# Optimization experiments

Measured on AMD Instinct MI355X. Metric: run time of the kernel, lower is better.

Reference implementation:

```python
import jax, jax.numpy as jnp
import numpy as np

NDIR = 6      # build_tree.num_directions()
IDIM = 256
ODIM = 512
B, L, NCH = 8, 4096, 8192


def setup_inputs() -> dict:
    key = jax.random.key(0)
    ks = jax.random.split(key, 9)
    last = jax.random.normal(ks[0], (B, NCH, IDIM), dtype=jnp.float32)
    child_l = jax.random.randint(ks[1], (L,), 0, NCH, dtype=jnp.int32)
    child_r = jax.random.randint(ks[2], (L,), 0, NCH, dtype=jnp.int32)
    vec = jax.random.randint(ks[3], (B, L), 0, NCH, dtype=jnp.int32)
    drev = jax.random.randint(ks[4], (NCH,), 0, 2, dtype=jnp.int32)
    dmap = jax.random.randint(ks[5], (NCH,), 0, NDIR, dtype=jnp.int32)
    # merge FC params: ndir independent Linear(2*idim -> odim) + PReLU(init=relu_weight)
    scale = 1.0 / np.sqrt(2 * IDIM)
    W_merge = jax.random.uniform(ks[6], (NDIR, ODIM, 2 * IDIM), jnp.float32, -scale, scale)
    b_merge = jax.random.uniform(ks[7], (NDIR, ODIM), jnp.float32, -scale, scale)
    alpha_merge = jnp.full((NDIR,), 0.005, dtype=jnp.float32)  # PReLU weight (relu_weight)
    return {"last": last, "W_merge": W_merge, "b_merge": b_merge,
            "alpha_merge": alpha_merge, "child_l": child_l, "child_r": child_r,
            "vec": vec, "drev": drev, "dmap": dmap}


def reference(last, W_merge, b_merge, alpha_merge, child_l, child_r, vec, drev, dmap):
    # child gathers: [B, L, idim]
    lch = last[:, child_l]
    rch = last[:, child_r]
    # per-element direction-reverse blending
    d = drev[vec][:, :, None].astype(last.dtype)          # [B, L, 1]
    a = lch * (1.0 - d) + rch * d
    b = rch * (1.0 - d) + lch * d
    ans = jnp.concatenate([a, b], axis=-1)                # [B, L, 2*idim]
    # routed merge: compute all ndir linears, then select per element (ndir is small)
    y_all = jnp.einsum('bli,doi->bldo', ans, W_merge) + b_merge   # [B, L, ndir, odim]
    dir_idx = dmap[vec]                                   # [B, L] in [0, ndir)
    y = jnp.take_along_axis(y_all, dir_idx[:, :, None, None], axis=2)[:, :, 0]  # [B, L, odim]
    alpha = alpha_merge[dir_idx][:, :, None]              # per-element PReLU slope
    return jnp.where(y > 0, y, alpha * y)
```

## Files before the change

### kernel.cpp

```cpp
#include <hip/hip_runtime.h>
#include <hip/hip_bf16.h>

#define BB 8
#define LL 4096
#define NCH 8192
#define IDIM 256
#define KDIM 512
#define ODIM 512
#define NDIR 6
#define TOT (BB * LL)

typedef short short8 __attribute__((ext_vector_type(8)));
typedef float floatx4 __attribute__((ext_vector_type(4)));

#define WS_LAST_OFF (64 + 2 * TOT)
#define LAST_ELEMS (BB * NCH * IDIM)
#define W_ELEMS (NDIR * ODIM * KDIM)
#define N_LAST8 (LAST_ELEMS / 8)
#define N_W8 (W_ELEMS / 8)

#define GEMM_CHUNK 131

__device__ inline void async_copy16(const void* g, void* l) {
  __builtin_amdgcn_global_load_lds(
      (const __attribute__((address_space(1))) void*)g,
      (__attribute__((address_space(3))) void*)l, 16, 0, 0);
}

__device__ inline void cvt8(const float* __restrict__ src,
                            __hip_bfloat16* __restrict__ dst, int i) {
  const floatx4* s = (const floatx4*)src;
  floatx4 a = s[2 * i];
  floatx4 b = s[2 * i + 1];
  union { short8 v; __hip_bfloat16 h[8]; } u;
  u.h[0] = __float2bfloat16(a[0]); u.h[1] = __float2bfloat16(a[1]);
  u.h[2] = __float2bfloat16(a[2]); u.h[3] = __float2bfloat16(a[3]);
  u.h[4] = __float2bfloat16(b[0]); u.h[5] = __float2bfloat16(b[1]);
  u.h[6] = __float2bfloat16(b[2]); u.h[7] = __float2bfloat16(b[3]);
  ((short8*)dst)[i] = u.v;
}

__global__ __launch_bounds__(256) void prep_kernel(
    const float* __restrict__ last, const float* __restrict__ W,
    const int* __restrict__ vec, const int* __restrict__ dmap,
    int* __restrict__ ws) {
  __hip_bfloat16* last_bf = (__hip_bfloat16*)(ws + WS_LAST_OFF);
  __hip_bfloat16* W_bf = last_bf + LAST_ELEMS;
  int gid = blockIdx.x * 256 + threadIdx.x;
  if (gid < N_LAST8) {
    cvt8(last, last_bf, gid);
  } else if (gid < N_LAST8 + N_W8) {
    cvt8(W, W_bf, gid - N_LAST8);
  } else {
    __shared__ int lcnt[8];
    int tid = threadIdx.x;
    if (tid < 8) lcnt[tid] = 0;
    __syncthreads();
    int lin = gid - (N_LAST8 + N_W8);
    int dir = dmap[vec[lin]] & 7;
    atomicAdd(&lcnt[dir], 1);
    __syncthreads();
    if (tid < 8 && lcnt[tid]) atomicAdd(&ws[tid], lcnt[tid]);
  }
}

__global__ __launch_bounds__(256) void scatter_kernel(
    const int* __restrict__ vec, const int* __restrict__ child_l,
    const int* __restrict__ child_r, const int* __restrict__ drev,
    const int* __restrict__ dmap, int* __restrict__ ws) {
  __shared__ int lcnt[8];
  __shared__ int gbase[8];
  __shared__ int baseS[8];
  int* fill = ws + 8;
  int* idx = ws + 64;
  int* rows = ws + 64 + TOT;

  int tid = threadIdx.x;
  if (tid < 8) {
    lcnt[tid] = 0;
    int s = 0;
    for (int i = 0; i < tid; ++i) s += ws[i];
    baseS[tid] = s;
  }
  __syncthreads();

  int lin = blockIdx.x * 256 + tid;
  int l = lin & (LL - 1);
  int v = vec[lin];
  int dir = dmap[v] & 7;
  int sw = drev[v];
  int cl = child_l[l];
  int cr = child_r[l];
  int r0 = sw ? cr : cl;
  int r1 = sw ? cl : cr;
  int pos = atomicAdd(&lcnt[dir], 1);
  __syncthreads();
  if (tid < 8) gbase[tid] = lcnt[tid] ? atomicAdd(&fill[tid], lcnt[tid]) : 0;
  __syncthreads();
  int slot = baseS[dir] + gbase[dir] + pos;
  idx[slot] = lin;
  rows[slot] = r0 | (r1 << 16);
}

__global__ __launch_bounds__(256) void gemm_kernel(
    const float* __restrict__ bias, const float* __restrict__ alpha_m,
    const int* __restrict__ ws, float* __restrict__ out) {
  __shared__ __hip_bfloat16 Als[2][128 * 64];

  int flat = blockIdx.y * 4 + blockIdx.x;
  int swz = (flat & 7) * GEMM_CHUNK + (flat >> 3);
  const int mt = swz >> 2;
  const int nt = swz & 3;

  int d = -1, count = 0, off = 0, m_base = 0;
  {
    int tb = 0, run = 0;
    for (int dd = 0; dd < NDIR; ++dd) {
      int c = ws[dd];
      int ntile = (c + 127) >> 7;
      if (mt < tb + ntile) { d = dd; count = c; off = run; m_base = (mt - tb) * 128; break; }
      tb += ntile; run += c;
    }
  }
  if (d < 0) return;

  const int* idx = ws + 64;
  const int* rows = ws + 64 + TOT;
  const __hip_bfloat16* last_bf = (const __hip_bfloat16*)(ws + WS_LAST_OFF);
  const __hip_bfloat16* W_bf = last_bf + LAST_ELEMS;

  const int tid = threadIdx.x;
  const int wave = __builtin_amdgcn_readfirstlane(tid >> 6);
  const int lane = tid & 63;
  const int lane15 = lane & 15;
  const int quad = lane >> 4;
  const int wm = wave >> 1;
  const int wn = wave & 1;
  const int n_blk = nt * 128;

  const __hip_bfloat16* ap0[4];
  const __hip_bfloat16* ap1[4];
  int ldsrow[4];
#pragma unroll
  for (int i = 0; i < 4; ++i) {
    int sr = wave * 32 + i * 8 + (lane >> 3);
    ldsrow[i] = (wave * 32 + i * 8) * 64;
    int lr = m_base + sr;
    if (lr >= count) lr = count - 1;
    int lin = idx[off + lr] & (TOT - 1);
    int rr = rows[off + lr];
    int b = lin >> 12;
    int r0 = rr & (NCH - 1);
    int r1 = (rr >> 16) & (NCH - 1);
    int xu = ((lane & 7) ^ (sr & 7)) * 8;
    ap0[i] = last_bf + (long long)(b * NCH + r0) * IDIM + xu;
    ap1[i] = last_bf + (long long)(b * NCH + r1) * IDIM + xu;
  }
  const __hip_bfloat16* bp[4];
#pragma unroll
  for (int j = 0; j < 4; ++j)
    bp[j] = W_bf + (long long)(d * ODIM + n_blk + wn * 64 + j * 16 + lane15) * KDIM + quad * 8;

  floatx4 acc[4][4] = {};
  const int lx = lane15 & 7;

#pragma unroll
  for (int i = 0; i < 4; ++i) async_copy16(ap0[i], &Als[0][ldsrow[i]]);
  __syncthreads();

#pragma unroll
  for (int kt = 0; kt < 8; ++kt) {
    const int cur = kt & 1;
    short8 bfr[2][4];
#pragma unroll
    for (int s = 0; s < 2; ++s)
#pragma unroll
      for (int j = 0; j < 4; ++j)
        bfr[s][j] = *(const short8*)(bp[j] + kt * 64 + s * 32);

    if (kt < 7) {
      const int tn = kt + 1;
      const int ko = (tn & 3) * 64;
#pragma unroll
      for (int i = 0; i < 4; ++i) {
        const __hip_bfloat16* ga = (tn < 4 ? ap0[i] : ap1[i]) + ko;
        async_copy16(ga, &Als[cur ^ 1][ldsrow[i]]);
      }
    }

#pragma unroll
    for (int s = 0; s < 2; ++s) {
      const int xcol = ((quad + 4 * s) ^ lx) * 8;
      short8 a[4];
#pragma unroll
      for (int i = 0; i < 4; ++i)
        a[i] = *(const short8*)&Als[cur][(wm * 64 + i * 16 + lane15) * 64 + xcol];
#pragma unroll
      for (int i = 0; i < 4; ++i)
#pragma unroll
        for (int j = 0; j < 4; ++j)
          acc[i][j] = __builtin_amdgcn_mfma_f32_16x16x32_bf16(a[i], bfr[s][j], acc[i][j], 0, 0, 0);
    }
    __syncthreads();
  }

  const float alpha = alpha_m[d];
  float bj[4];
#pragma unroll
  for (int j = 0; j < 4; ++j)
    bj[j] = bias[d * ODIM + n_blk + wn * 64 + j * 16 + lane15];

#pragma unroll
  for (int i = 0; i < 4; ++i) {
#pragma unroll
    for (int reg = 0; reg < 4; ++reg) {
      int row_id = m_base + wm * 64 + i * 16 + quad * 4 + reg;
      if (row_id >= count) continue;
      int lin = idx[off + row_id] & (TOT - 1);
      float* orow = out + (long long)lin * ODIM + n_blk + wn * 64;
#pragma unroll
      for (int j = 0; j < 4; ++j) {
        float y = acc[i][j][reg] + bj[j];
        y = y > 0.f ? y : alpha * y;
        orow[j * 16 + lane15] = y;
      }
    }
  }
}

extern "C" void kernel_launch(void* const* d_in, const int* in_sizes, int n_in,
                              void* d_out, int out_size, void* d_ws, size_t ws_size,
                              hipStream_t stream) {
  const float* last = (const float*)d_in[0];
  const float* W = (const float*)d_in[1];
  const float* bias = (const float*)d_in[2];
  const float* alpha = (const float*)d_in[3];
  const int* child_l = (const int*)d_in[4];
  const int* child_r = (const int*)d_in[5];
  const int* vec = (const int*)d_in[6];
  const int* drev = (const int*)d_in[7];
  const int* dmap = (const int*)d_in[8];

  int* ws = (int*)d_ws;

  hipMemsetAsync(ws, 0, 64 * sizeof(int), stream);
  int prep_blocks = (N_LAST8 + N_W8 + TOT) / 256;
  prep_kernel<<<prep_blocks, 256, 0, stream>>>(last, W, vec, dmap, ws);
  scatter_kernel<<<TOT / 256, 256, 0, stream>>>(vec, child_l, child_r, drev, dmap, ws);
  dim3 grid(ODIM / 128, TOT / 128 + NDIR, 1);
  gemm_kernel<<<grid, 256, 0, stream>>>(bias, alpha, ws, (float*)d_out);
}
```

Baseline: 184.2 us.

## Fuse scatter into prep with per-direction buckets and use single-wave GEMM tiles

Drops the separate scatter kernel by having prep directly write index/row pairs into fixed-capacity per-direction buckets (CAP slots each), so no prefix sum over counts is needed. The GEMM switches to 64-thread single-wave blocks computing 64x64 tiles, with explicit s_waitcnt-based double buffering in place of __syncthreads. The aim is to save a launch and barrier overhead and to get more, smaller tiles for load balance. In exchange each tile reuses less data, and the code assumes no direction ever exceeds CAP entries.

```diff
diff --git a/kernel.cpp b/kernel.cpp
--- a/kernel.cpp
+++ b/kernel.cpp
@@ -10,16 +10,18 @@
 #define NDIR 6
 #define TOT (BB * LL)
 
-typedef short short8 __attribute__((ext_vector_type(8)));
-typedef float floatx4 __attribute__((ext_vector_type(4)));
-
-#define WS_LAST_OFF (64 + 2 * TOT)
+#define CAP 8192
+#define IDX_OFF 64
+#define ROWS_OFF (64 + 8 * CAP)
+#define WS_LAST_OFF (64 + 16 * CAP)
 #define LAST_ELEMS (BB * NCH * IDIM)
 #define W_ELEMS (NDIR * ODIM * KDIM)
 #define N_LAST8 (LAST_ELEMS / 8)
 #define N_W8 (W_ELEMS / 8)
 
-#define GEMM_CHUNK 131
+#define MTILES (TOT / 64 + NDIR)
+typedef short short8 __attribute__((ext_vector_type(8)));
+typedef float floatx4 __attribute__((ext_vector_type(4)));
 
 __device__ inline void async_copy16(const void* g, void* l) {
   __builtin_amdgcn_global_load_lds(
@@ -42,8 +44,9 @@
 
 __global__ __launch_bounds__(256) void prep_kernel(
     const float* __restrict__ last, const float* __restrict__ W,
-    const int* __restrict__ vec, const int* __restrict__ dmap,
-    int* __restrict__ ws) {
+    const int* __restrict__ vec, const int* __restrict__ child_l,
+    const int* __restrict__ child_r, const int* __restrict__ drev,
+    const int* __restrict__ dmap, int* __restrict__ ws) {
   __hip_bfloat16* last_bf = (__hip_bfloat16*)(ws + WS_LAST_OFF);
   __hip_bfloat16* W_bf = last_bf + LAST_ELEMS;
   int gid = blockIdx.x * 256 + threadIdx.x;
@@ -53,140 +56,107 @@
     cvt8(W, W_bf, gid - N_LAST8);
   } else {
     __shared__ int lcnt[8];
+    __shared__ int gbase[8];
     int tid = threadIdx.x;
     if (tid < 8) lcnt[tid] = 0;
     __syncthreads();
     int lin = gid - (N_LAST8 + N_W8);
-    int dir = dmap[vec[lin]] & 7;
-    atomicAdd(&lcnt[dir], 1);
+    int l = lin & (LL - 1);
+    int v = vec[lin];
+    int dir = dmap[v] & 7;
+    int sw = drev[v];
+    int cl = child_l[l];
+    int cr = child_r[l];
+    int r0 = sw ? cr : cl;
+    int r1 = sw ? cl : cr;
+    int pos = atomicAdd(&lcnt[dir], 1);
     __syncthreads();
-    if (tid < 8 && lcnt[tid]) atomicAdd(&ws[tid], lcnt[tid]);
-  }
-}
-
-__global__ __launch_bounds__(256) void scatter_kernel(
-    const int* __restrict__ vec, const int* __restrict__ child_l,
-    const int* __restrict__ child_r, const int* __restrict__ drev,
-    const int* __restrict__ dmap, int* __restrict__ ws) {
-  __shared__ int lcnt[8];
-  __shared__ int gbase[8];
-  __shared__ int baseS[8];
-  int* fill = ws + 8;
-  int* idx = ws + 64;
-  int* rows = ws + 64 + TOT;
-
-  int tid = threadIdx.x;
-  if (tid < 8) {
-    lcnt[tid] = 0;
-    int s = 0;
-    for (int i = 0; i < tid; ++i) s += ws[i];
-    baseS[tid] = s;
-  }
-  __syncthreads();
-
-  int lin = blockIdx.x * 256 + tid;
-  int l = lin & (LL - 1);
-  int v = vec[lin];
-  int dir = dmap[v] & 7;
-  int sw = drev[v];
-  int cl = child_l[l];
-  int cr = child_r[l];
-  int r0 = sw ? cr : cl;
-  int r1 = sw ? cl : cr;
-  int pos = atomicAdd(&lcnt[dir], 1);
-  __syncthreads();
-  if (tid < 8) gbase[tid] = lcnt[tid] ? atomicAdd(&fill[tid], lcnt[tid]) : 0;
-  __syncthreads();
-  int slot = baseS[dir] + gbase[dir] + pos;
-  idx[slot] = lin;
-  rows[slot] = r0 | (r1 << 16);
-}
-
-__global__ __launch_bounds__(256) void gemm_kernel(
+    if (tid < 8) gbase[tid] = lcnt[tid] ? atomicAdd(&ws[tid], lcnt[tid]) : 0;
+    __syncthreads();
+    int slot = dir * CAP + gbase[dir] + pos;
+    ws[IDX_OFF + slot] = lin;
+    ws[ROWS_OFF + slot] = r0 | (r1 << 16);
+  }
+}
+
+__global__ __launch_bounds__(64) void gemm_kernel(
     const float* __restrict__ bias, const float* __restrict__ alpha_m,
     const int* __restrict__ ws, float* __restrict__ out) {
-  __shared__ __hip_bfloat16 Als[2][128 * 64];
-
-  int flat = blockIdx.y * 4 + blockIdx.x;
-  int swz = (flat & 7) * GEMM_CHUNK + (flat >> 3);
-  const int mt = swz >> 2;
-  const int nt = swz & 3;
-
-  int d = -1, count = 0, off = 0, m_base = 0;
+  __shared__ __hip_bfloat16 Als[2][64 * 64];
+
+  int flat = blockIdx.y * 8 + blockIdx.x;
+  int swz = (flat & 7) * MTILES + (flat >> 3);
+  const int mt = swz >> 3;
+  const int nt = swz & 7;
+
+  int d = -1, count = 0, m_base = 0;
   {
-    int tb = 0, run = 0;
-    for (int dd = 0; dd < NDIR; ++dd) {
+    int tb = 0;
+    for (int dd = 0; dd < 8; ++dd) {
       int c = ws[dd];
-      int ntile = (c + 127) >> 7;
-      if (mt < tb + ntile) { d = dd; count = c; off = run; m_base = (mt - tb) * 128; break; }
-      tb += ntile; run += c;
+      int ntile = (c + 63) >> 6;
+      if (mt < tb + ntile) { d = dd; count = c; m_base = (mt - tb) * 64; break; }
+      tb += ntile;
     }
   }
   if (d < 0) return;
 
-  const int* idx = ws + 64;
-  const int* rows = ws + 64 + TOT;
-  const __hip_bfloat16* last_bf = (const __hip_bfloat16*)(ws + WS_LAST_OFF);
-  const __hip_bfloat16* W_bf = last_bf + LAST_ELEMS;
-
-  const int tid = threadIdx.x;
-  const int wave = __builtin_amdgcn_readfirstlane(tid >> 6);
-  const int lane = tid & 63;
+  const int* idxA = ws + IDX_OFF + d * CAP;
+  const int* rowsA = ws + ROWS_OFF + d * CAP;
+  const char* last_bf = (const char*)(ws + WS_LAST_OFF);
+  const char* W_bf = last_bf + (long long)LAST_ELEMS * 2;
+
+  const int lane = threadIdx.x;
   const int lane15 = lane & 15;
   const int quad = lane >> 4;
-  const int wm = wave >> 1;
-  const int wn = wave & 1;
-  const int n_blk = nt * 128;
-
-  const __hip_bfloat16* ap0[4];
-  const __hip_bfloat16* ap1[4];
-  int ldsrow[4];
-#pragma unroll
-  for (int i = 0; i < 4; ++i) {
-    int sr = wave * 32 + i * 8 + (lane >> 3);
-    ldsrow[i] = (wave * 32 + i * 8) * 64;
-    int lr = m_base + sr;
-    if (lr >= count) lr = count - 1;
-    int lin = idx[off + lr] & (TOT - 1);
-    int rr = rows[off + lr];
+
+  int aoff0[8], aoff1[8];
+  const int xu2 = (((lane & 7) ^ (lane >> 3)) * 8) * 2;
+#pragma unroll
+  for (int i = 0; i < 8; ++i) {
+    int gr = m_base + i * 8 + (lane >> 3);
+    if (gr >= count) gr = count - 1;
+    int lin = idxA[gr] & (TOT - 1);
+    int rr = rowsA[gr];
     int b = lin >> 12;
-    int r0 = rr & (NCH - 1);
-    int r1 = (rr >> 16) & (NCH - 1);
-    int xu = ((lane & 7) ^ (sr & 7)) * 8;
-    ap0[i] = last_bf + (long long)(b * NCH + r0) * IDIM + xu;
-    ap1[i] = last_bf + (long long)(b * NCH + r1) * IDIM + xu;
-  }
-  const __hip_bfloat16* bp[4];
+    aoff0[i] = (b * NCH + (rr & (NCH - 1))) * (IDIM * 2) + xu2;
+    aoff1[i] = (b * NCH + ((rr >> 16) & (NCH - 1))) * (IDIM * 2) + xu2;
+  }
+  int boff[4];
 #pragma unroll
   for (int j = 0; j < 4; ++j)
-    bp[j] = W_bf + (long long)(d * ODIM + n_blk + wn * 64 + j * 16 + lane15) * KDIM + quad * 8;
+    boff[j] = ((d * ODIM + nt * 64 + j * 16 + lane15) * KDIM + quad * 8) * 2;
 
   floatx4 acc[4][4] = {};
   const int lx = lane15 & 7;
 
 #pragma unroll
-  for (int i = 0; i < 4; ++i) async_copy16(ap0[i], &Als[0][ldsrow[i]]);
-  __syncthreads();
-
-#pragma unroll
-  for (int kt = 0; kt < 8; ++kt) {
-    const int cur = kt & 1;
+  for (int i = 0; i < 8; ++i)
+    async_copy16(last_bf + aoff0[i], &Als[0][i * 512]);
+
+#pragma unroll
+  for (int t = 0; t < 8; ++t) {
+    const int cur = t & 1;
     short8 bfr[2][4];
 #pragma unroll
     for (int s = 0; s < 2; ++s)
 #pragma unroll
       for (int j = 0; j < 4; ++j)
-        bfr[s][j] = *(const short8*)(bp[j] + kt * 64 + s * 32);
-
-    if (kt < 7) {
-      const int tn = kt + 1;
-      const int ko = (tn & 3) * 64;
-#pragma unroll
-      for (int i = 0; i < 4; ++i) {
-        const __hip_bfloat16* ga = (tn < 4 ? ap0[i] : ap1[i]) + ko;
-        async_copy16(ga, &Als[cur ^ 1][ldsrow[i]]);
-      }
-    }
+        bfr[s][j] = *(const short8*)(W_bf + boff[j] + (t * 64 + s * 32) * 2);
+
+    asm volatile("s_waitcnt lgkmcnt(0)" ::: "memory");
+    if (t < 7) {
+      const int tn = t + 1;
+      const int ko = (tn & 3) * (64 * 2);
+#pragma unroll
+      for (int i = 0; i < 8; ++i)
+        async_copy16(last_bf + (tn < 4 ? aoff0[i] : aoff1[i]) + ko,
+                     &Als[cur ^ 1][i * 512]);
+      asm volatile("s_waitcnt vmcnt(8)" ::: "memory");
+    } else {
+      asm volatile("s_waitcnt vmcnt(0)" ::: "memory");
+    }
+    __builtin_amdgcn_sched_barrier(0);
 
 #pragma unroll
     for (int s = 0; s < 2; ++s) {
@@ -194,30 +164,29 @@
       short8 a[4];
 #pragma unroll
       for (int i = 0; i < 4; ++i)
-        a[i] = *(const short8*)&Als[cur][(wm * 64 + i * 16 + lane15) * 64 + xcol];
+        a[i] = *(const short8*)&Als[cur][(i * 16 + lane15) * 64 + xcol];
 #pragma unroll
       for (int i = 0; i < 4; ++i)
 #pragma unroll
         for (int j = 0; j < 4; ++j)
           acc[i][j] = __builtin_amdgcn_mfma_f32_16x16x32_bf16(a[i], bfr[s][j], acc[i][j], 0, 0, 0);
     }
-    __syncthreads();
   }
 
   const float alpha = alpha_m[d];
   float bj[4];
 #pragma unroll
   for (int j = 0; j < 4; ++j)
-    bj[j] = bias[d * ODIM + n_blk + wn * 64 + j * 16 + lane15];
+    bj[j] = bias[d * ODIM + nt * 64 + j * 16 + lane15];
 
 #pragma unroll
   for (int i = 0; i < 4; ++i) {
 #pragma unroll
     for (int reg = 0; reg < 4; ++reg) {
-      int row_id = m_base + wm * 64 + i * 16 + quad * 4 + reg;
+      int row_id = m_base + i * 16 + quad * 4 + reg;
       if (row_id >= count) continue;
-      int lin = idx[off + row_id] & (TOT - 1);
-      float* orow = out + (long long)lin * ODIM + n_blk + wn * 64;
+      int lin = idxA[row_id] & (TOT - 1);
+      float* orow = out + (long long)lin * ODIM + nt * 64;
 #pragma unroll
       for (int j = 0; j < 4; ++j) {
         float y = acc[i][j][reg] + bj[j];
@@ -244,9 +213,9 @@
   int* ws = (int*)d_ws;
 
   hipMemsetAsync(ws, 0, 64 * sizeof(int), stream);
-  int prep_blocks = (N_LAST8 + N_W8 + TOT) / 256;
-  prep_kernel<<<prep_blocks, 256, 0, stream>>>(last, W, vec, dmap, ws);
-  scatter_kernel<<<TOT / 256, 256, 0, stream>>>(vec, child_l, child_r, drev, dmap, ws);
-  dim3 grid(ODIM / 128, TOT / 128 + NDIR, 1);
-  gemm_kernel<<<grid, 256, 0, stream>>>(bias, alpha, ws, (float*)d_out);
-}
+  int prep_blocks = N_LAST8 / 256 + N_W8 / 256 + TOT / 256;
+  prep_kernel<<<prep_blocks, 256, 0, stream>>>(last, W, vec, child_l, child_r,
+                                               drev, dmap, ws);
+  dim3 grid(8, MTILES, 1);
+  gemm_kernel<<<grid, 64, 0, stream>>>(bias, alpha, ws, (float*)d_out);
+}
```

Result: no change. 182.8 us (-0.7%).
